# Kernel tuning notes

Measured on AMD Instinct MI355X. Metric: run time of the kernel, lower is better.

Reference implementation:

```python
import jax, jax.numpy as jnp
import numpy as np

EPS = 1e-6
NUM_HEADS = 24

def _rmsnorm(x, w):
    # x: [..., D], fp32 math as in FluxRMSNorm
    xf = x.astype(jnp.float32)
    inv = jax.lax.rsqrt(jnp.mean(xf * xf, axis=-1, keepdims=True) + EPS)
    return w * (xf * inv).astype(x.dtype)

def setup_inputs() -> dict:
    key = jax.random.key(0)
    ks = jax.random.split(key, 4)
    B, N, H = 1, 2048, 3072
    D = H // NUM_HEADS
    s_in = 1.0 / np.sqrt(H)
    return {
        "x": jax.random.normal(ks[0], (B, N, H), jnp.float32),
        "Wqkv": jax.random.normal(ks[1], (H, 3 * H), jnp.float32) * s_in,
        "b_qkv": jnp.zeros((3 * H,), jnp.float32),
        "Wproj": jax.random.normal(ks[2], (H, H), jnp.float32) * s_in,
        "q_norm_w": jnp.ones((D,), jnp.float32),
        "k_norm_w": jnp.ones((D,), jnp.float32),
    }

def reference(x, Wqkv, b_qkv, Wproj, q_norm_w, k_norm_w):
    B, N, hidden = x.shape
    nh = NUM_HEADS
    hd = hidden // nh
    scale = hd ** (-0.5)
    qkv = (x @ Wqkv + b_qkv).reshape(B, N, 3, nh, hd)
    q, k, v = qkv[:, :, 0], qkv[:, :, 1], qkv[:, :, 2]  # [B,N,nh,hd]
    q = _rmsnorm(q, q_norm_w)
    k = _rmsnorm(k, k_norm_w)
    # scores: [B,nh,N,N]
    scores = jnp.einsum('bqhd,bkhd->bhqk', q, k) * scale
    attn = jax.nn.softmax(scores, axis=-1)
    out = jnp.einsum('bhqk,bkhd->bqhd', attn, v).reshape(B, N, hidden)
    return out @ Wproj
```

## Files before the change

### kernel.cpp

```cpp
#include <hip/hip_runtime.h>
#include <hip/hip_bf16.h>

using bf16 = __hip_bfloat16;
typedef __attribute__((ext_vector_type(8))) short short8;
typedef __attribute__((ext_vector_type(4))) float f32x4;
typedef unsigned long long ull;

static constexpr int SEQ  = 2048;
static constexpr int HID  = 3072;
static constexpr int NH   = 24;
static constexpr int HD   = 128;
static constexpr int QKVN = 9216;

__device__ __forceinline__ f32x4 mfma_16x16x32(short8 a, short8 b, f32x4 c) {
  return __builtin_amdgcn_mfma_f32_16x16x32_bf16(a, b, c, 0, 0, 0);
}

#define GLOAD_LDS16(g, l) __builtin_amdgcn_global_load_lds(                 \
    (const __attribute__((address_space(1))) void*)(g),                    \
    (__attribute__((address_space(3))) void*)(l), 16, 0, 0)

typedef __attribute__((address_space(3))) const unsigned char lds_cchar;

__global__ __launch_bounds__(256)
void cvt_f32_bf16_vec(const float* __restrict__ src, bf16* __restrict__ dst, int n4) {
  int i = blockIdx.x * 256 + threadIdx.x;
  if (i >= n4) return;
  float4 v = ((const float4*)src)[i];
  ushort4 o;
  bf16 t0 = __float2bfloat16(v.x); o.x = *(unsigned short*)&t0;
  bf16 t1 = __float2bfloat16(v.y); o.y = *(unsigned short*)&t1;
  bf16 t2 = __float2bfloat16(v.z); o.z = *(unsigned short*)&t2;
  bf16 t3 = __float2bfloat16(v.w); o.w = *(unsigned short*)&t3;
  ((ushort4*)dst)[i] = o;
}

__global__ __launch_bounds__(256)
void transpose_cvt64(const float* __restrict__ src, bf16* __restrict__ dst, int R, int C) {
  __shared__ float tile[32][65];
  const int c0 = blockIdx.x * 64, r0 = blockIdx.y * 32;
  const int lc = threadIdx.x & 63, lt = threadIdx.x >> 6;
  #pragma unroll
  for (int i = 0; i < 8; ++i)
    tile[lt + i * 4][lc] = src[(size_t)(r0 + lt + i * 4) * C + c0 + lc];
  __syncthreads();
  const int u = threadIdx.x & 15, dr = threadIdx.x >> 4;
  #pragma unroll
  for (int j = 0; j < 4; ++j) {
    const int cc = dr + j * 16;
    bf16 x0 = __float2bfloat16(tile[u * 2][cc]);
    bf16 x1 = __float2bfloat16(tile[u * 2 + 1][cc]);
    ushort2 o;
    o.x = *(unsigned short*)&x0; o.y = *(unsigned short*)&x1;
    *(ushort2*)&dst[(size_t)(c0 + cc) * R + r0 + u * 2] = o;
  }
}

template<int BIAS>
__global__ __launch_bounds__(768, 3)
void gemm12w(const bf16* __restrict__ A, const bf16* __restrict__ BT,
             const float* __restrict__ bias, bf16* __restrict__ Cout,
             int M, int N, int K) {
  __shared__ __align__(16) bf16 Asb[2][256 * 64];
  __shared__ __align__(16) bf16 Bsb[2][288 * 64];

  const int tid  = threadIdx.x;
  const int lane = tid & 63;
  const int wid  = tid >> 6;
  const int wm   = wid / 6;
  const int wn   = wid % 6;
  const int lr   = lane & 15;
  const int lg   = lane >> 4;

  const int bm = (blockIdx.x & 7) * 256;
  const int bn = (blockIdx.x >> 3) * 288;

  const int lrow = lane >> 3;
  const int csrc = ((lane & 7) ^ lrow) * 8;
  const bf16* Abase = A  + (size_t)(bm + lrow) * K + csrc;
  const bf16* Bbase = BT + (size_t)(bn + lrow) * K + csrc;

#define STG12(b, u, i) do {                                                       \
    const int L_ = wid + 12 * (i);                                                \
    if (L_ < 32)      GLOAD_LDS16(Abase + (size_t)(8 * L_) * K + (size_t)(u) * 64,\
                                  &Asb[b][L_ * 512]);                             \
    else if (L_ < 68) GLOAD_LDS16(Bbase + (size_t)(8 * (L_ - 32)) * K + (size_t)(u) * 64, \
                                  &Bsb[b][(L_ - 32) * 512]);                      \
  } while (0)
#define RA12(b, m, kk) (*(const short8*)(&Asb[b][(wm * 128 + (m) * 16 + lr) * 64 \
                          + ((((kk) * 4 + lg)) ^ (lr & 7)) * 8]))
#define RB12(b, n, kk) (*(const short8*)(&Bsb[b][(wn * 48 + (n) * 16 + lr) * 64 \
                          + ((((kk) * 4 + lg)) ^ (lr & 7)) * 8]))

  f32x4 acc[8][3] = {};
  const int NT = K >> 6;

  #pragma unroll
  for (int i = 0; i < 6; ++i) STG12(0, 0, i);

  for (int t = 0; t < NT; ++t) {
    const int c = t & 1, nc = c ^ 1;
    const bool pf = (t + 1) < NT;
    short8 a[4], b[3];

    asm volatile("s_waitcnt vmcnt(0)" ::: "memory");
    __builtin_amdgcn_s_barrier();

    if (pf) { STG12(nc, t + 1, 0); STG12(nc, t + 1, 1); STG12(nc, t + 1, 2); }
    __builtin_amdgcn_sched_barrier(0);
    b[0] = RB12(c, 0, 0); b[1] = RB12(c, 1, 0); b[2] = RB12(c, 2, 0);
    a[0] = RA12(c, 0, 0); a[1] = RA12(c, 1, 0); a[2] = RA12(c, 2, 0); a[3] = RA12(c, 3, 0);
    __builtin_amdgcn_s_setprio(1);
    #pragma unroll
    for (int n = 0; n < 3; ++n)
      #pragma unroll
      for (int m = 0; m < 4; ++m) acc[m][n] = mfma_16x16x32(a[m], b[n], acc[m][n]);
    __builtin_amdgcn_s_setprio(0);
    __builtin_amdgcn_s_barrier();

    if (pf) { STG12(nc, t + 1, 3); STG12(nc, t + 1, 4); STG12(nc, t + 1, 5); }
    __builtin_amdgcn_sched_barrier(0);
    a[0] = RA12(c, 4, 0); a[1] = RA12(c, 5, 0); a[2] = RA12(c, 6, 0); a[3] = RA12(c, 7, 0);
    __builtin_amdgcn_s_setprio(1);
    #pragma unroll
    for (int n = 0; n < 3; ++n)
      #pragma unroll
      for (int m = 0; m < 4; ++m) acc[4 + m][n] = mfma_16x16x32(a[m], b[n], acc[4 + m][n]);
    __builtin_amdgcn_s_setprio(0);
    __builtin_amdgcn_s_barrier();

    b[0] = RB12(c, 0, 1); b[1] = RB12(c, 1, 1); b[2] = RB12(c, 2, 1);
    a[0] = RA12(c, 0, 1); a[1] = RA12(c, 1, 1); a[2] = RA12(c, 2, 1); a[3] = RA12(c, 3, 1);
    __builtin_amdgcn_s_setprio(1);
    #pragma unroll
    for (int n = 0; n < 3; ++n)
      #pragma unroll
      for (int m = 0; m < 4; ++m) acc[m][n] = mfma_16x16x32(a[m], b[n], acc[m][n]);
    __builtin_amdgcn_s_setprio(0);
    __builtin_amdgcn_s_barrier();

    a[0] = RA12(c, 4, 1); a[1] = RA12(c, 5, 1); a[2] = RA12(c, 6, 1); a[3] = RA12(c, 7, 1);
    __builtin_amdgcn_s_setprio(1);
    #pragma unroll
    for (int n = 0; n < 3; ++n)
      #pragma unroll
      for (int m = 0; m < 4; ++m) acc[4 + m][n] = mfma_16x16x32(a[m], b[n], acc[4 + m][n]);
    __builtin_amdgcn_s_setprio(0);
  }
#undef STG12
#undef RA12
#undef RB12

  const int row0 = bm + wm * 128 + lg * 4;
  const int col0 = bn + wn * 48 + lr;
  #pragma unroll
  for (int n = 0; n < 3; ++n) {
    const int col = col0 + n * 16;
    const float bv = BIAS ? bias[col] : 0.0f;
    #pragma unroll
    for (int m = 0; m < 8; ++m)
      #pragma unroll
      for (int r = 0; r < 4; ++r)
        Cout[(size_t)(row0 + m * 16 + r) * N + col] = __float2bfloat16(acc[m][n][r] + bv);
  }
}

__global__ __launch_bounds__(512, 2)
void gemm8w(const bf16* __restrict__ A, const bf16* __restrict__ BT,
            float* __restrict__ Cout, int M, int N, int K) {
  __shared__ __align__(16) bf16 Asb[2][128 * 64];
  __shared__ __align__(16) bf16 Bsb[2][192 * 64];

  const int tid  = threadIdx.x;
  const int lane = tid & 63;
  const int wid  = tid >> 6;
  const int wm   = wid >> 2;
  const int wn   = wid & 3;
  const int lr   = lane & 15;
  const int lg   = lane >> 4;

  const int bm = (2 * (blockIdx.x & 7) + ((blockIdx.x >> 3) & 1)) * 128;
  const int bn = (blockIdx.x >> 4) * 192;

  const int lrow = lane >> 3;
  const int csrc = ((lane & 7) ^ lrow) * 8;
  const bf16* Abase = A  + (size_t)(bm + lrow) * K + csrc;
  const bf16* Bbase = BT + (size_t)(bn + lrow) * K + csrc;

#define STG8(b, u, i) do {                                                        \
    const int L_ = wid + 8 * (i);                                                 \
    if (L_ < 16)      GLOAD_LDS16(Abase + (size_t)(8 * L_) * K + (size_t)(u) * 64,\
                                  &Asb[b][L_ * 512]);                             \
    else              GLOAD_LDS16(Bbase + (size_t)(8 * (L_ - 16)) * K + (size_t)(u) * 64, \
                                  &Bsb[b][(L_ - 16) * 512]);                      \
  } while (0)
#define RA8(b, m, kk) (*(const short8*)(&Asb[b][(wm * 64 + (m) * 16 + lr) * 64 \
                          + ((((kk) * 4 + lg)) ^ (lr & 7)) * 8]))
#define RB8(b, n, kk) (*(const short8*)(&Bsb[b][(wn * 48 + (n) * 16 + lr) * 64 \
                          + ((((kk) * 4 + lg)) ^ (lr & 7)) * 8]))

  f32x4 acc[4][3] = {};
  const int NT = K >> 6;

  #pragma unroll
  for (int i = 0; i < 5; ++i) STG8(0, 0, i);

  for (int t = 0; t < NT; ++t) {
    const int c = t & 1, nc = c ^ 1;
    const bool pf = (t + 1) < NT;
    short8 a[4], b[3];

    asm volatile("s_waitcnt vmcnt(0)" ::: "memory");
    __builtin_amdgcn_s_barrier();

    if (pf) { STG8(nc, t + 1, 0); STG8(nc, t + 1, 1); STG8(nc, t + 1, 2); }
    __builtin_amdgcn_sched_barrier(0);
    b[0] = RB8(c, 0, 0); b[1] = RB8(c, 1, 0); b[2] = RB8(c, 2, 0);
    a[0] = RA8(c, 0, 0); a[1] = RA8(c, 1, 0); a[2] = RA8(c, 2, 0); a[3] = RA8(c, 3, 0);
    __builtin_amdgcn_s_setprio(1);
    #pragma unroll
    for (int n = 0; n < 3; ++n)
      #pragma unroll
      for (int m = 0; m < 4; ++m) acc[m][n] = mfma_16x16x32(a[m], b[n], acc[m][n]);
    __builtin_amdgcn_s_setprio(0);
    __builtin_amdgcn_s_barrier();

    if (pf) { STG8(nc, t + 1, 3); STG8(nc, t + 1, 4); }
    __builtin_amdgcn_sched_barrier(0);
    b[0] = RB8(c, 0, 1); b[1] = RB8(c, 1, 1); b[2] = RB8(c, 2, 1);
    a[0] = RA8(c, 0, 1); a[1] = RA8(c, 1, 1); a[2] = RA8(c, 2, 1); a[3] = RA8(c, 3, 1);
    __builtin_amdgcn_s_setprio(1);
    #pragma unroll
    for (int n = 0; n < 3; ++n)
      #pragma unroll
      for (int m = 0; m < 4; ++m) acc[m][n] = mfma_16x16x32(a[m], b[n], acc[m][n]);
    __builtin_amdgcn_s_setprio(0);
  }
#undef STG8
#undef RA8
#undef RB8

  const int row0 = bm + wm * 64 + lg * 4;
  const int col0 = bn + wn * 48 + lr;
  #pragma unroll
  for (int n = 0; n < 3; ++n) {
    const int col = col0 + n * 16;
    #pragma unroll
    for (int m = 0; m < 4; ++m)
      #pragma unroll
      for (int r = 0; r < 4; ++r)
        Cout[(size_t)(row0 + m * 16 + r) * N + col] = acc[m][n][r];
  }
}

__global__ __launch_bounds__(256)
void rmsnorm_qk(bf16* __restrict__ qkv, const float* __restrict__ qw,
                const float* __restrict__ kw) {
  const int row  = blockIdx.x * 4 + (threadIdx.x >> 6);
  const int lane = threadIdx.x & 63;
  const int token = row / 48;
  const int rem   = row - token * 48;
  const int which = rem / 24;
  const int head  = rem - which * 24;
  bf16* p = qkv + (long)token * QKVN + which * HID + head * HD;
  const float a = __bfloat162float(p[lane * 2]);
  const float b = __bfloat162float(p[lane * 2 + 1]);
  float ss = a * a + b * b;
  #pragma unroll
  for (int mask = 32; mask >= 1; mask >>= 1) ss += __shfl_xor(ss, mask);
  const float inv = rsqrtf(ss * (1.0f / 128.0f) + 1e-6f);
  const float* w = which ? kw : qw;
  p[lane * 2]     = __float2bfloat16(a * inv * w[lane * 2]);
  p[lane * 2 + 1] = __float2bfloat16(b * inv * w[lane * 2 + 1]);
}

__global__ __launch_bounds__(256, 2)
void attn_kernel(const bf16* __restrict__ qkv, bf16* __restrict__ ctx) {
  const int head = blockIdx.y;
  const int qb   = blockIdx.x;
  const int tid  = threadIdx.x;
  const int lane = tid & 63;
  const int wid  = tid >> 6;
  const int lr   = lane & 15;
  const int lg   = lane >> 4;

  __shared__ __align__(16) unsigned char Ksb[64 * 256];
  __shared__ __align__(16) unsigned char Vsb[128 * 128];
  __shared__ __align__(16) unsigned short Ps[4][16 * 72];

  const int qrow0 = qb * 64 + wid * 16;
  short8 qf[4];
  #pragma unroll
  for (int kt = 0; kt < 4; ++kt)
    qf[kt] = *(const short8*)(qkv + (long)(qrow0 + lr) * QKVN + head * HD + kt * 32 + lg * 8);

  f32x4 oacc[8] = {};
  float mrun[4], lrun[4];
  #pragma unroll
  for (int r = 0; r < 4; ++r) { mrun[r] = -1e30f; lrun[r] = 0.0f; }

  const float scale = 0.088388347648318447f;

  for (int t = 0; t < SEQ / 64; ++t) {
    const int kv0 = t * 64;
    short8 kreg[4], vreg[4];
    int tokv[4], dchv[4];
    #pragma unroll
    for (int j = 0; j < 4; ++j) {
      const int id  = tid + j * 256;
      const int tok = id >> 4;
      const int dc  = id & 15;
      tokv[j] = tok; dchv[j] = dc;
      kreg[j] = *(const short8*)(qkv + (long)(kv0 + tok) * QKVN + HID     + head * HD + dc * 8);
      vreg[j] = *(const short8*)(qkv + (long)(kv0 + tok) * QKVN + 2 * HID + head * HD + dc * 8);
    }
    __syncthreads();
    #pragma unroll
    for (int j = 0; j < 4; ++j) {
      const int tok = tokv[j], dc = dchv[j];
      *(short8*)(Ksb + ((tok * 256 + dc * 16) ^ ((tok & 7) << 4))) = kreg[j];
      const int dg = dc >> 1, h = dc & 1, kg = tok >> 2, kr = tok & 3;
      const int pos = (kg & 8) | ((kg & 1) << 2) | ((kg >> 1) & 3);
      *(short8*)(Vsb + (dg * 16 + pos) * 128 + kr * 32 + h * 16) = vreg[j];
    }
    __syncthreads();

    f32x4 s[4];
    __builtin_amdgcn_s_setprio(1);
    #pragma unroll
    for (int ct = 0; ct < 4; ++ct) {
      f32x4 a = {};
      #pragma unroll
      for (int kt = 0; kt < 4; ++kt) {
        short8 kb = *(const short8*)(Ksb +
            ((((ct * 16 + lr) * 256) + kt * 64 + lg * 16) ^ ((lr & 7) << 4)));
        a = mfma_16x16x32(qf[kt], kb, a);
      }
      s[ct] = a;
    }
    __builtin_amdgcn_s_setprio(0);

    #pragma unroll
    for (int r = 0; r < 4; ++r) {
      float pm = fmaxf(fmaxf(s[0][r], s[1][r]), fmaxf(s[2][r], s[3][r]));
      #pragma unroll
      for (int mask = 1; mask <= 8; mask <<= 1) pm = fmaxf(pm, __shfl_xor(pm, mask));
      pm *= scale;
      const float mnew = fmaxf(mrun[r], pm);
      const float corr = __expf(mrun[r] - mnew);
      float psum = 0.0f;
      #pragma unroll
      for (int ct = 0; ct < 4; ++ct) {
        const float p = __expf(s[ct][r] * scale - mnew);
        psum += p;
        bf16 pb = __float2bfloat16(p);
        Ps[wid][(lg * 4 + r) * 72 + ct * 16 + lr] = *(unsigned short*)&pb;
      }
      #pragma unroll
      for (int mask = 1; mask <= 8; mask <<= 1) psum += __shfl_xor(psum, mask);
      lrun[r] = lrun[r] * corr + psum;
      mrun[r] = mnew;
      #pragma unroll
      for (int dt = 0; dt < 8; ++dt) oacc[dt][r] *= corr;
    }

    short8 pa[2];
    #pragma unroll
    for (int kt = 0; kt < 2; ++kt)
      pa[kt] = *(const short8*)&Ps[wid][lr * 72 + kt * 32 + lg * 8];

    lds_cchar* vb0 = (lds_cchar*)Vsb + lane * 8;
    __builtin_amdgcn_s_setprio(1);
    #pragma unroll
    for (int dt = 0; dt < 8; ++dt) {
      lds_cchar* pd = vb0 + dt * 2048;
      ull r0, r1, r2, r3;
      asm volatile("ds_read_b64_tr_b16 %0, %1 offset:0"    : "=v"(r0) : "v"(pd));
      asm volatile("ds_read_b64_tr_b16 %0, %1 offset:512"  : "=v"(r1) : "v"(pd));
      asm volatile("ds_read_b64_tr_b16 %0, %1 offset:1024" : "=v"(r2) : "v"(pd));
      asm volatile("ds_read_b64_tr_b16 %0, %1 offset:1536" : "=v"(r3) : "v"(pd));
      asm volatile("s_waitcnt lgkmcnt(0)" ::: "memory");
      __builtin_amdgcn_sched_barrier(0);
      short8 vb_0, vb_1;
      ((ull*)&vb_0)[0] = r0; ((ull*)&vb_0)[1] = r1;
      ((ull*)&vb_1)[0] = r2; ((ull*)&vb_1)[1] = r3;
      oacc[dt] = mfma_16x16x32(pa[0], vb_0, oacc[dt]);
      oacc[dt] = mfma_16x16x32(pa[1], vb_1, oacc[dt]);
    }
    __builtin_amdgcn_s_setprio(0);
  }

  #pragma unroll
  for (int r = 0; r < 4; ++r) {
    const float inv = 1.0f / lrun[r];
    const long tok = qrow0 + lg * 4 + r;
    #pragma unroll
    for (int dt = 0; dt < 8; ++dt)
      ctx[tok * HID + head * HD + dt * 16 + lr] = __float2bfloat16(oacc[dt][r] * inv);
  }
}

extern "C" void kernel_launch(void* const* d_in, const int* in_sizes, int n_in,
                              void* d_out, int out_size, void* d_ws, size_t ws_size,
                              hipStream_t stream) {
  (void)in_sizes; (void)n_in; (void)out_size; (void)ws_size;
  const float* x     = (const float*)d_in[0];
  const float* Wqkv  = (const float*)d_in[1];
  const float* bqkv  = (const float*)d_in[2];
  const float* Wproj = (const float*)d_in[3];
  const float* qw    = (const float*)d_in[4];
  const float* kw    = (const float*)d_in[5];

  char* ws = (char*)d_ws;
  bf16* xb     = (bf16*)ws;
  bf16* WqkvT  = (bf16*)(ws + 12582912);
  bf16* WprojT = (bf16*)(ws + 69206016);
  bf16* qkv    = (bf16*)(ws + 88080384);
  bf16* ctx    = xb;

  cvt_f32_bf16_vec<<<(SEQ * HID / 4 + 255) / 256, 256, 0, stream>>>(x, xb, SEQ * HID / 4);
  transpose_cvt64<<<dim3(QKVN / 64, HID / 32), 256, 0, stream>>>(Wqkv, WqkvT, HID, QKVN);
  transpose_cvt64<<<dim3(HID / 64, HID / 32), 256, 0, stream>>>(Wproj, WprojT, HID, HID);

  gemm12w<1><<<256, 768, 0, stream>>>(xb, WqkvT, bqkv, qkv, SEQ, QKVN, HID);

  rmsnorm_qk<<<SEQ * 48 / 4, 256, 0, stream>>>(qkv, qw, kw);

  attn_kernel<<<dim3(SEQ / 64, NH), 256, 0, stream>>>(qkv, ctx);

  gemm8w<<<256, 512, 0, stream>>>(ctx, WprojT, (float*)d_out, SEQ, HID, HID);
}
```

Before: 379.2 us.

## Prefetch next KV tile into registers in attention; simplify GEMM main-loop barriers

```diff
diff --git a/kernel.cpp b/kernel.cpp
--- a/kernel.cpp
+++ b/kernel.cpp
@@ -106,46 +106,37 @@
     asm volatile("s_waitcnt vmcnt(0)" ::: "memory");
     __builtin_amdgcn_s_barrier();
 
-    if (pf) { STG12(nc, t + 1, 0); STG12(nc, t + 1, 1); STG12(nc, t + 1, 2); }
+    if (pf) {
+      STG12(nc, t + 1, 0); STG12(nc, t + 1, 1); STG12(nc, t + 1, 2);
+      STG12(nc, t + 1, 3); STG12(nc, t + 1, 4); STG12(nc, t + 1, 5);
+    }
     __builtin_amdgcn_sched_barrier(0);
+
     b[0] = RB12(c, 0, 0); b[1] = RB12(c, 1, 0); b[2] = RB12(c, 2, 0);
     a[0] = RA12(c, 0, 0); a[1] = RA12(c, 1, 0); a[2] = RA12(c, 2, 0); a[3] = RA12(c, 3, 0);
-    __builtin_amdgcn_s_setprio(1);
     #pragma unroll
     for (int n = 0; n < 3; ++n)
       #pragma unroll
       for (int m = 0; m < 4; ++m) acc[m][n] = mfma_16x16x32(a[m], b[n], acc[m][n]);
-    __builtin_amdgcn_s_setprio(0);
-    __builtin_amdgcn_s_barrier();
-
-    if (pf) { STG12(nc, t + 1, 3); STG12(nc, t + 1, 4); STG12(nc, t + 1, 5); }
-    __builtin_amdgcn_sched_barrier(0);
+
     a[0] = RA12(c, 4, 0); a[1] = RA12(c, 5, 0); a[2] = RA12(c, 6, 0); a[3] = RA12(c, 7, 0);
-    __builtin_amdgcn_s_setprio(1);
     #pragma unroll
     for (int n = 0; n < 3; ++n)
       #pragma unroll
       for (int m = 0; m < 4; ++m) acc[4 + m][n] = mfma_16x16x32(a[m], b[n], acc[4 + m][n]);
-    __builtin_amdgcn_s_setprio(0);
-    __builtin_amdgcn_s_barrier();
 
     b[0] = RB12(c, 0, 1); b[1] = RB12(c, 1, 1); b[2] = RB12(c, 2, 1);
     a[0] = RA12(c, 0, 1); a[1] = RA12(c, 1, 1); a[2] = RA12(c, 2, 1); a[3] = RA12(c, 3, 1);
-    __builtin_amdgcn_s_setprio(1);
     #pragma unroll
     for (int n = 0; n < 3; ++n)
       #pragma unroll
       for (int m = 0; m < 4; ++m) acc[m][n] = mfma_16x16x32(a[m], b[n], acc[m][n]);
-    __builtin_amdgcn_s_setprio(0);
-    __builtin_amdgcn_s_barrier();
 
     a[0] = RA12(c, 4, 1); a[1] = RA12(c, 5, 1); a[2] = RA12(c, 6, 1); a[3] = RA12(c, 7, 1);
-    __builtin_amdgcn_s_setprio(1);
     #pragma unroll
     for (int n = 0; n < 3; ++n)
       #pragma unroll
       for (int m = 0; m < 4; ++m) acc[4 + m][n] = mfma_16x16x32(a[m], b[n], acc[4 + m][n]);
-    __builtin_amdgcn_s_setprio(0);
   }
 #undef STG12
 #undef RA12
@@ -213,28 +204,25 @@
     asm volatile("s_waitcnt vmcnt(0)" ::: "memory");
     __builtin_amdgcn_s_barrier();
 
-    if (pf) { STG8(nc, t + 1, 0); STG8(nc, t + 1, 1); STG8(nc, t + 1, 2); }
+    if (pf) {
+      STG8(nc, t + 1, 0); STG8(nc, t + 1, 1); STG8(nc, t + 1, 2);
+      STG8(nc, t + 1, 3); STG8(nc, t + 1, 4);
+    }
     __builtin_amdgcn_sched_barrier(0);
+
     b[0] = RB8(c, 0, 0); b[1] = RB8(c, 1, 0); b[2] = RB8(c, 2, 0);
     a[0] = RA8(c, 0, 0); a[1] = RA8(c, 1, 0); a[2] = RA8(c, 2, 0); a[3] = RA8(c, 3, 0);
-    __builtin_amdgcn_s_setprio(1);
     #pragma unroll
     for (int n = 0; n < 3; ++n)
       #pragma unroll
       for (int m = 0; m < 4; ++m) acc[m][n] = mfma_16x16x32(a[m], b[n], acc[m][n]);
-    __builtin_amdgcn_s_setprio(0);
-    __builtin_amdgcn_s_barrier();
-
-    if (pf) { STG8(nc, t + 1, 3); STG8(nc, t + 1, 4); }
-    __builtin_amdgcn_sched_barrier(0);
+
     b[0] = RB8(c, 0, 1); b[1] = RB8(c, 1, 1); b[2] = RB8(c, 2, 1);
     a[0] = RA8(c, 0, 1); a[1] = RA8(c, 1, 1); a[2] = RA8(c, 2, 1); a[3] = RA8(c, 3, 1);
-    __builtin_amdgcn_s_setprio(1);
     #pragma unroll
     for (int n = 0; n < 3; ++n)
       #pragma unroll
       for (int m = 0; m < 4; ++m) acc[m][n] = mfma_16x16x32(a[m], b[n], acc[m][n]);
-    __builtin_amdgcn_s_setprio(0);
   }
 #undef STG8
 #undef RA8
@@ -301,29 +289,41 @@
 
   const float scale = 0.088388347648318447f;
 
+  const int stok = tid >> 4;
+  const int sdc  = tid & 15;
+
+  short8 kreg[4], vreg[4];
+  #pragma unroll
+  for (int j = 0; j < 4; ++j) {
+    const int tok = stok + (j & 1) * 16 + (j >> 1) * 32;
+    const int dc  = sdc;
+    kreg[j] = *(const short8*)(qkv + (long)tok * QKVN + HID     + head * HD + dc * 8);
+    vreg[j] = *(const short8*)(qkv + (long)tok * QKVN + 2 * HID + head * HD + dc * 8);
+  }
+
   for (int t = 0; t < SEQ / 64; ++t) {
-    const int kv0 = t * 64;
-    short8 kreg[4], vreg[4];
-    int tokv[4], dchv[4];
+    __syncthreads();
     #pragma unroll
     for (int j = 0; j < 4; ++j) {
-      const int id  = tid + j * 256;
-      const int tok = id >> 4;
-      const int dc  = id & 15;
-      tokv[j] = tok; dchv[j] = dc;
-      kreg[j] = *(const short8*)(qkv + (long)(kv0 + tok) * QKVN + HID     + head * HD + dc * 8);
-      vreg[j] = *(const short8*)(qkv + (long)(kv0 + tok) * QKVN + 2 * HID + head * HD + dc * 8);
-    }
-    __syncthreads();
-    #pragma unroll
-    for (int j = 0; j < 4; ++j) {
-      const int tok = tokv[j], dc = dchv[j];
+      const int tok = stok + (j & 1) * 16 + (j >> 1) * 32;
+      const int dc  = sdc;
       *(short8*)(Ksb + ((tok * 256 + dc * 16) ^ ((tok & 7) << 4))) = kreg[j];
       const int dg = dc >> 1, h = dc & 1, kg = tok >> 2, kr = tok & 3;
       const int pos = (kg & 8) | ((kg & 1) << 2) | ((kg >> 1) & 3);
       *(short8*)(Vsb + (dg * 16 + pos) * 128 + kr * 32 + h * 16) = vreg[j];
     }
     __syncthreads();
+
+    if (t + 1 < SEQ / 64) {
+      const int kv1 = (t + 1) * 64;
+      #pragma unroll
+      for (int j = 0; j < 4; ++j) {
+        const int tok = kv1 + stok + (j & 1) * 16 + (j >> 1) * 32;
+        kreg[j] = *(const short8*)(qkv + (long)tok * QKVN + HID     + head * HD + sdc * 8);
+        vreg[j] = *(const short8*)(qkv + (long)tok * QKVN + 2 * HID + head * HD + sdc * 8);
+      }
+      __builtin_amdgcn_sched_barrier(0);
+    }
 
     f32x4 s[4];
     __builtin_amdgcn_s_setprio(1);
```

Measured after the change: 355.6 us. 1.07x faster.
